# Performance work log

Measured on AMD Instinct MI355X. Metric: run time of the kernel, lower is better.

Reference implementation:

```python
import jax, jax.numpy as jnp
import numpy as np

V, H_BASE, D, L, K = 32000, 4096, 512, 2, 4
B = 64

def setup_inputs() -> dict:
    key = jax.random.key(0)
    ks = jax.random.split(key, 12)
    s = 0.02
    return {
        "hidden_state": jax.random.normal(ks[0], (B, H_BASE), jnp.float32),
        "in_proj_w": jax.random.normal(ks[1], (D, H_BASE), jnp.float32) * s,
        "in_proj_b": jnp.zeros((D,), jnp.float32),
        "w_ih0": jax.random.normal(ks[2], (3 * D, D), jnp.float32) * s,
        "w_hh0": jax.random.normal(ks[3], (3 * D, D), jnp.float32) * s,
        "b_ih0": jax.random.normal(ks[4], (3 * D,), jnp.float32) * s,
        "b_hh0": jax.random.normal(ks[5], (3 * D,), jnp.float32) * s,
        "w_ih1": jax.random.normal(ks[6], (3 * D, D), jnp.float32) * s,
        "w_hh1": jax.random.normal(ks[7], (3 * D, D), jnp.float32) * s,
        "b_ih1": jax.random.normal(ks[8], (3 * D,), jnp.float32) * s,
        "b_hh1": jax.random.normal(ks[9], (3 * D,), jnp.float32) * s,
        "embed": jax.random.normal(ks[10], (V, D), jnp.float32) * s,
        "out_w": jax.random.normal(ks[11], (V, D), jnp.float32) * s,
    }

def _gru_cell(x, h, w_ih, w_hh, b_ih, b_hh):
    # PyTorch GRU gate order: r, z, n
    gi = x @ w_ih.T + b_ih  # [B, 3D]
    gh = h @ w_hh.T + b_hh
    ir, iz, inn = jnp.split(gi, 3, axis=-1)
    hr, hz, hn = jnp.split(gh, 3, axis=-1)
    r = jax.nn.sigmoid(ir + hr)
    z = jax.nn.sigmoid(iz + hz)
    n = jnp.tanh(inn + r * hn)
    return (1.0 - z) * n + z * h

def reference(hidden_state, in_proj_w, in_proj_b, w_ih0, w_hh0, b_ih0, b_hh0,
              w_ih1, w_hh1, b_ih1, b_hh1, embed, out_w):
    b = hidden_state.shape[0]
    h0 = hidden_state @ in_proj_w.T + in_proj_b  # [B, D]
    h_l0 = h0
    h_l1 = h0
    x = jnp.zeros((b, in_proj_w.shape[0]), hidden_state.dtype)
    all_logits = []
    for _ in range(K):
        h_l0 = _gru_cell(x, h_l0, w_ih0, w_hh0, b_ih0, b_hh0)
        h_l1 = _gru_cell(h_l0, h_l1, w_ih1, w_hh1, b_ih1, b_hh1)
        logits = h_l1 @ out_w.T  # [B, V]
        all_logits.append(logits)
        x = embed[jnp.argmax(logits, axis=-1)]  # greedy next-token embed
    return jnp.stack(all_logits, axis=1)  # [B, K, V]
```

## Files before the change

kernel.cpp:

```cpp
#include <hip/hip_runtime.h>
#include <math.h>


typedef __attribute__((ext_vector_type(8))) short short8;
typedef __attribute__((ext_vector_type(4))) float f32x4;

__device__ __forceinline__ unsigned short f2bf_rne(float x) {
    unsigned u = __float_as_uint(x);
    unsigned r = (u + 0x7fffu + ((u >> 16) & 1u)) >> 16;
    return (unsigned short)r;
}
__device__ __forceinline__ void split2(float x, unsigned short& hi, unsigned short& lo) {
    unsigned u = __float_as_uint(x);
    hi = (unsigned short)(u >> 16);
    float r = x - __uint_as_float(u & 0xffff0000u);
    lo = f2bf_rne(r);
}

__device__ __forceinline__ void store_plane(unsigned short* hiP, unsigned short* loP,
                                            int m, int d, float v) {
    int s = d >> 6, cl = (d >> 3) & 7, e = d & 7;
    int off = m * 512 + s * 64 + ((cl ^ (m & 7)) * 8) + e;
    unsigned short hi, lo; split2(v, hi, lo);
    hiP[off] = hi; loP[off] = lo;
}

__device__ __forceinline__ void gload16(const void* g, void* lds) {
    __builtin_amdgcn_global_load_lds(
        (const __attribute__((address_space(1))) unsigned int*)g,
        (__attribute__((address_space(3))) unsigned int*)lds, 16, 0, 0);
}

#define LDTB 72

template<bool ARGMAX>
__device__ __forceinline__ void mfma_gemm(
    const char* __restrict__ AH, const char* __restrict__ AL, int AstrideB,
    const float* __restrict__ W, int ldbK,
    int n0, int k0, int klen,
    float* __restrict__ C, int ldc,
    unsigned short* AsH, unsigned short* AsL,
    unsigned short* BsH, unsigned short* BsL,
    float* __restrict__ pval, int* __restrict__ pidx, int bx)
{
    const int tid  = threadIdx.x;
    const int wv   = tid >> 6;
    const int lane = tid & 63;
    const int lr   = lane & 15;
    const int lh   = lane >> 4;

    f32x4 acc[4];
#pragma unroll
    for (int i = 0; i < 4; ++i) acc[i] = (f32x4){0.f, 0.f, 0.f, 0.f};

    for (int kk = k0; kk < k0 + klen; kk += 64) {
        {
            int m  = tid >> 3;
            int cp = tid & 7;
            const char* sH = AH + m * AstrideB + kk * 2 + cp * 16;
            const char* sL = AL + m * AstrideB + kk * 2 + cp * 16;
            gload16(sH, (char*)AsH + wv * 1024);
            gload16(sL, (char*)AsL + wv * 1024);
        }
#pragma unroll
        for (int r = 0; r < 4; ++r) {
            int idx = r * 512 + tid;
            int n = idx >> 4;
            int q = idx & 15;
            float4 v = *(const float4*)(W + (n0 + n) * ldbK + kk + q * 4);
            unsigned short h0,h1,h2,h3,l0,l1,l2,l3;
            split2(v.x,h0,l0); split2(v.y,h1,l1); split2(v.z,h2,l2); split2(v.w,h3,l3);
            uint2 ph = make_uint2((unsigned)h0 | ((unsigned)h1 << 16),
                                  (unsigned)h2 | ((unsigned)h3 << 16));
            uint2 pl = make_uint2((unsigned)l0 | ((unsigned)l1 << 16),
                                  (unsigned)l2 | ((unsigned)l3 << 16));
            *(uint2*)(BsH + n * LDTB + q * 4) = ph;
            *(uint2*)(BsL + n * LDTB + q * 4) = pl;
        }
        __syncthreads();

#pragma unroll
        for (int kk2 = 0; kk2 < 2; ++kk2) {
            int aoff = lr * 64 + (((kk2 * 4 + lh) ^ (lr & 7)) * 8);
            short8 ah[4], al[4];
#pragma unroll
            for (int mt = 0; mt < 4; ++mt) {
                ah[mt] = *(const short8*)(AsH + mt * 1024 + aoff);
                al[mt] = *(const short8*)(AsL + mt * 1024 + aoff);
            }
            int boff = (wv * 16 + lr) * LDTB + kk2 * 32 + lh * 8;
            short8 bh = *(const short8*)(BsH + boff);
            short8 bl = *(const short8*)(BsL + boff);
#pragma unroll
            for (int mt = 0; mt < 4; ++mt) {
                acc[mt] = __builtin_amdgcn_mfma_f32_16x16x32_bf16(ah[mt], bh, acc[mt], 0, 0, 0);
                acc[mt] = __builtin_amdgcn_mfma_f32_16x16x32_bf16(ah[mt], bl, acc[mt], 0, 0, 0);
                acc[mt] = __builtin_amdgcn_mfma_f32_16x16x32_bf16(al[mt], bh, acc[mt], 0, 0, 0);
            }
        }
        __syncthreads();
    }

#pragma unroll
    for (int mt = 0; mt < 4; ++mt)
#pragma unroll
        for (int i = 0; i < 4; ++i) {
            int m = mt * 16 + lh * 4 + i;
            C[m * ldc + n0 + wv * 16 + lr] = acc[mt][i];
        }

    if (ARGMAX) {
        float* sv = (float*)AsH;
        int*   sc = (int*)AsL;
#pragma unroll
        for (int mt = 0; mt < 4; ++mt)
#pragma unroll
            for (int i = 0; i < 4; ++i) {
                float v = acc[mt][i];
                int   c = n0 + wv * 16 + lr;
#pragma unroll
                for (int msk = 1; msk < 16; msk <<= 1) {
                    float ov = __shfl_xor(v, msk, 64);
                    int   oc = __shfl_xor(c, msk, 64);
                    if (ov > v || (ov == v && oc < c)) { v = ov; c = oc; }
                }
                if (lr == 0) {
                    int row = mt * 16 + lh * 4 + i;
                    sv[wv * 64 + row] = v;
                    sc[wv * 64 + row] = c;
                }
            }
        __syncthreads();
        if (tid < 64) {
            float v = sv[tid]; int c = sc[tid];
#pragma unroll
            for (int w = 1; w < 8; ++w) {
                float ov = sv[w * 64 + tid]; int oc = sc[w * 64 + tid];
                if (ov > v) { v = ov; c = oc; }
            }
            pval[bx * 64 + tid] = v;
            pidx[bx * 64 + tid] = c;
        }
    }
}

#define DECLARE_LDS() \
    __shared__ alignas(16) unsigned short AsH[64 * 64]; \
    __shared__ alignas(16) unsigned short AsL[64 * 64]; \
    __shared__ alignas(16) unsigned short BsH[128 * LDTB]; \
    __shared__ alignas(16) unsigned short BsL[128 * LDTB];

__global__ __launch_bounds__(256) void k_split_A(
    const float* __restrict__ hidden, char* __restrict__ hidH, char* __restrict__ hidL)
{
    int g = blockIdx.x * 256 + threadIdx.x;
    int m = g >> 9;
    int cc = g & 511;
    int s = cc >> 3, cl = cc & 7;
    const float* src = hidden + m * 4096 + cc * 8;
    float4 v0 = *(const float4*)src;
    float4 v1 = *(const float4*)(src + 4);
    unsigned short h[8], l[8];
    split2(v0.x,h[0],l[0]); split2(v0.y,h[1],l[1]); split2(v0.z,h[2],l[2]); split2(v0.w,h[3],l[3]);
    split2(v1.x,h[4],l[4]); split2(v1.y,h[5],l[5]); split2(v1.z,h[6],l[6]); split2(v1.w,h[7],l[7]);
    uint4 ph = make_uint4((unsigned)h[0]|((unsigned)h[1]<<16), (unsigned)h[2]|((unsigned)h[3]<<16),
                          (unsigned)h[4]|((unsigned)h[5]<<16), (unsigned)h[6]|((unsigned)h[7]<<16));
    uint4 pl = make_uint4((unsigned)l[0]|((unsigned)l[1]<<16), (unsigned)l[2]|((unsigned)l[3]<<16),
                          (unsigned)l[4]|((unsigned)l[5]<<16), (unsigned)l[6]|((unsigned)l[7]<<16));
    int off = m * 8192 + s * 128 + ((cl ^ (m & 7)) * 16);
    *(uint4*)(hidH + off) = ph;
    *(uint4*)(hidL + off) = pl;
}

__global__ __launch_bounds__(512) void k_inproj(
    const char* __restrict__ hidH, const char* __restrict__ hidL,
    const float* __restrict__ W, float* __restrict__ part)
{
    DECLARE_LDS();
    int nt = blockIdx.x & 3;
    int ks = blockIdx.x >> 2;
    mfma_gemm<false>(hidH, hidL, 8192, W, 4096, nt * 128, ks * 512, 512,
                     part + ks * 32768, 512, AsH, AsL, BsH, BsL, nullptr, nullptr, 0);
}

__global__ __launch_bounds__(256) void k_reduce_inproj(
    const float* __restrict__ part, const float* __restrict__ bias,
    float* __restrict__ hA, float* __restrict__ hB,
    unsigned short* hAH, unsigned short* hAL,
    unsigned short* hBH, unsigned short* hBL,
    unsigned short* xH,  unsigned short* xL)
{
    int i = blockIdx.x * 256 + threadIdx.x;
    int b = i >> 9;
    int d = i & 511;
    float s = bias[d];
#pragma unroll
    for (int ks = 0; ks < 8; ++ks) s += part[ks * 32768 + i];
    hA[i] = s;
    hB[i] = s;
    store_plane(hAH, hAL, b, d, s);
    store_plane(hBH, hBL, b, d, s);
    store_plane(xH,  xL,  b, d, 0.f);
}

__global__ __launch_bounds__(512) void k_gates(
    const char* __restrict__ xH, const char* __restrict__ xL,
    const char* __restrict__ hH, const char* __restrict__ hL,
    const float* __restrict__ w_ih, const float* __restrict__ w_hh,
    float* __restrict__ gip, float* __restrict__ ghp)
{
    DECLARE_LDS();
    int bx = blockIdx.x;
    int nt = bx % 12;
    int ks = (bx / 12) & 1;
    int mat = bx / 24;
    const char* AH = mat ? hH : xH;
    const char* AL = mat ? hL : xL;
    const float* W = mat ? w_hh : w_ih;
    float* C = (mat ? ghp : gip) + ks * 98304;
    mfma_gemm<false>(AH, AL, 1024, W, 512, nt * 128, ks * 256, 256, C, 1536,
                     AsH, AsL, BsH, BsL, nullptr, nullptr, 0);
}

__global__ __launch_bounds__(256) void k_combine(
    const float* __restrict__ gip, const float* __restrict__ ghp,
    const float* __restrict__ b_ih, const float* __restrict__ b_hh,
    float* __restrict__ h, unsigned short* hH, unsigned short* hL)
{
    int i = blockIdx.x * 256 + threadIdx.x;
    int b = i >> 9;
    int d = i & 511;
    int base = b * 1536 + d;
    float ir = gip[base]         + gip[98304 + base]         + b_ih[d];
    float iz = gip[base + 512]   + gip[98304 + base + 512]   + b_ih[d + 512];
    float inn= gip[base + 1024]  + gip[98304 + base + 1024]  + b_ih[d + 1024];
    float hr = ghp[base]         + ghp[98304 + base]         + b_hh[d];
    float hz = ghp[base + 512]   + ghp[98304 + base + 512]   + b_hh[d + 512];
    float hn = ghp[base + 1024]  + ghp[98304 + base + 1024]  + b_hh[d + 1024];
    float r = 1.f / (1.f + expf(-(ir + hr)));
    float z = 1.f / (1.f + expf(-(iz + hz)));
    float n = tanhf(inn + r * hn);
    float hv = (1.f - z) * n + z * h[i];
    h[i] = hv;
    store_plane(hH, hL, b, d, hv);
}

__global__ __launch_bounds__(512) void k_logits(
    const char* __restrict__ hH, const char* __restrict__ hL,
    const float* __restrict__ W, float* __restrict__ out, int step,
    float* __restrict__ pval, int* __restrict__ pidx)
{
    DECLARE_LDS();
    mfma_gemm<true>(hH, hL, 1024, W, 512, blockIdx.x * 128, 0, 512,
                    out + step * 32000, 128000, AsH, AsL, BsH, BsL,
                    pval, pidx, blockIdx.x);
}

__global__ __launch_bounds__(256) void k_reduce_embed(
    const float* __restrict__ pval, const int* __restrict__ pidx,
    const float* __restrict__ embed, unsigned short* xH, unsigned short* xL)
{
    __shared__ float sv[256];
    __shared__ int   sc[256];
    const int b = blockIdx.x;
    const int tid = threadIdx.x;
    float v = -3.4e38f;
    int   c = 0x7fffffff;
    if (tid < 250) { v = pval[tid * 64 + b]; c = pidx[tid * 64 + b]; }
    sv[tid] = v; sc[tid] = c;
    __syncthreads();
    for (int s = 128; s > 0; s >>= 1) {
        if (tid < s) {
            float ov = sv[tid + s]; int oc = sc[tid + s];
            if (ov > sv[tid] || (ov == sv[tid] && oc < sc[tid])) { sv[tid] = ov; sc[tid] = oc; }
        }
        __syncthreads();
    }
    int tok = sc[0];
    for (int j = tid; j < 512; j += 256)
        store_plane(xH, xL, b, j, embed[tok * 512 + j]);
}

extern "C" void kernel_launch(void* const* d_in, const int* in_sizes, int n_in,
                              void* d_out, int out_size, void* d_ws, size_t ws_size,
                              hipStream_t stream)
{
    const float* hidden = (const float*)d_in[0];
    const float* in_w   = (const float*)d_in[1];
    const float* in_b   = (const float*)d_in[2];
    const float* w_ih0  = (const float*)d_in[3];
    const float* w_hh0  = (const float*)d_in[4];
    const float* b_ih0  = (const float*)d_in[5];
    const float* b_hh0  = (const float*)d_in[6];
    const float* w_ih1  = (const float*)d_in[7];
    const float* w_hh1  = (const float*)d_in[8];
    const float* b_ih1  = (const float*)d_in[9];
    const float* b_hh1  = (const float*)d_in[10];
    const float* embed  = (const float*)d_in[11];
    const float* out_w  = (const float*)d_in[12];
    float* out = (float*)d_out;
    char*  ws  = (char*)d_ws;

    float* hA  = (float*)(ws + 0);
    float* hB  = (float*)(ws + 131072);
    unsigned short* xH  = (unsigned short*)(ws + 262144);
    unsigned short* xL  = (unsigned short*)(ws + 327680);
    unsigned short* hAH = (unsigned short*)(ws + 393216);
    unsigned short* hAL = (unsigned short*)(ws + 458752);
    unsigned short* hBH = (unsigned short*)(ws + 524288);
    unsigned short* hBL = (unsigned short*)(ws + 589824);
    char* hidH = ws + 655360;
    char* hidL = ws + 1179648;
    float* gip = (float*)(ws + 1703936);
    float* ghp = (float*)(ws + 2490368);
    float* ipart = gip;
    float* pval = (float*)(ws + 3276800);
    int*   pidx = (int*)  (ws + 3340800);

    k_split_A<<<128, 256, 0, stream>>>(hidden, hidH, hidL);
    k_inproj<<<32, 512, 0, stream>>>(hidH, hidL, in_w, ipart);
    k_reduce_inproj<<<128, 256, 0, stream>>>(ipart, in_b, hA, hB,
                                             hAH, hAL, hBH, hBL, xH, xL);

    for (int step = 0; step < 4; ++step) {
        k_gates<<<48, 512, 0, stream>>>((char*)xH, (char*)xL, (char*)hAH, (char*)hAL,
                                        w_ih0, w_hh0, gip, ghp);
        k_combine<<<128, 256, 0, stream>>>(gip, ghp, b_ih0, b_hh0, hA, hAH, hAL);
        k_gates<<<48, 512, 0, stream>>>((char*)hAH, (char*)hAL, (char*)hBH, (char*)hBL,
                                        w_ih1, w_hh1, gip, ghp);
        k_combine<<<128, 256, 0, stream>>>(gip, ghp, b_ih1, b_hh1, hB, hBH, hBL);
        k_logits<<<250, 512, 0, stream>>>((char*)hBH, (char*)hBL, out_w, out, step, pval, pidx);
        k_reduce_embed<<<64, 256, 0, stream>>>(pval, pidx, embed, xH, xL);
    }
}
```

Measured before the change: 383.7 us.

## Pre-split weights into bf16 hi/lo tiled planes and double-buffer async loads

Adds kernels that split every weight matrix (out_w, GRU weights, in_proj) into bf16 hi/lo planes once per call, stored in a pre-tiled swizzled layout. The GEMM then loads B tiles straight into LDS with async global_load_lds, in a two-stage double buffer alongside the A tiles, instead of splitting fp32 in registers on every step. The split-K factor is doubled for the GRU gates and in_proj to raise block counts. The cost is an extra upfront pass writing about 2x the weight bytes each call. After that, every logits step reads 64 MB of bf16 planes instead of 64 MB of fp32, so traffic is not reduced, only the conversion work.

```diff
diff --git a/kernel.cpp b/kernel.cpp
--- a/kernel.cpp
+++ b/kernel.cpp
@@ -31,16 +31,59 @@
         (__attribute__((address_space(3))) unsigned int*)lds, 16, 0, 0);
 }
 
-#define LDTB 72
+__device__ __forceinline__ void split_w_body(
+    const float* __restrict__ W, unsigned short* __restrict__ H,
+    unsigned short* __restrict__ L, size_t g, int kclog)
+{
+    int n  = (int)(g >> kclog);
+    int c8 = (int)g & ((1 << kclog) - 1);
+    const float* src = W + g * 8;
+    float4 v0 = *(const float4*)src;
+    float4 v1 = *(const float4*)(src + 4);
+    unsigned short h[8], l[8];
+    split2(v0.x,h[0],l[0]); split2(v0.y,h[1],l[1]); split2(v0.z,h[2],l[2]); split2(v0.w,h[3],l[3]);
+    split2(v1.x,h[4],l[4]); split2(v1.y,h[5],l[5]); split2(v1.z,h[6],l[6]); split2(v1.w,h[7],l[7]);
+    uint4 ph = make_uint4((unsigned)h[0]|((unsigned)h[1]<<16), (unsigned)h[2]|((unsigned)h[3]<<16),
+                          (unsigned)h[4]|((unsigned)h[5]<<16), (unsigned)h[6]|((unsigned)h[7]<<16));
+    uint4 pl = make_uint4((unsigned)l[0]|((unsigned)l[1]<<16), (unsigned)l[2]|((unsigned)l[3]<<16),
+                          (unsigned)l[4]|((unsigned)l[5]<<16), (unsigned)l[6]|((unsigned)l[7]<<16));
+    int nt = n >> 7, row = n & 127;
+    int ksi = c8 >> 3;
+    int slot = (c8 & 7) ^ (row & 7);
+    int tpr = 1 << (kclog - 3);
+    size_t off = ((size_t)(nt * tpr + ksi) * 128 + row) * 64 + slot * 8;
+    *(uint4*)(H + off) = ph;
+    *(uint4*)(L + off) = pl;
+}
+
+__global__ __launch_bounds__(256) void k_split_W(
+    const float* __restrict__ W, unsigned short* __restrict__ H,
+    unsigned short* __restrict__ L, int kclog)
+{
+    size_t g = (size_t)blockIdx.x * 256 + threadIdx.x;
+    split_w_body(W, H, L, g, kclog);
+}
+
+__global__ __launch_bounds__(256) void k_split_gw(
+    const float* __restrict__ w0, const float* __restrict__ w1,
+    const float* __restrict__ w2, const float* __restrict__ w3,
+    unsigned short* __restrict__ H, unsigned short* __restrict__ L)
+{
+    int mat = blockIdx.y;
+    const float* W = mat == 0 ? w0 : mat == 1 ? w1 : mat == 2 ? w2 : w3;
+    size_t g = (size_t)blockIdx.x * 256 + threadIdx.x;
+    split_w_body(W, H + (size_t)mat * 786432, L + (size_t)mat * 786432, g, 6);
+}
 
 template<bool ARGMAX>
 __device__ __forceinline__ void mfma_gemm(
-    const char* __restrict__ AH, const char* __restrict__ AL, int AstrideB,
-    const float* __restrict__ W, int ldbK,
-    int n0, int k0, int klen,
-    float* __restrict__ C, int ldc,
-    unsigned short* AsH, unsigned short* AsL,
-    unsigned short* BsH, unsigned short* BsL,
+    const char* __restrict__ AH, const char* __restrict__ AL, int AstrideB, int akk0,
+    const unsigned short* __restrict__ BH, const unsigned short* __restrict__ BL,
+    size_t btileU,
+    int nk,
+    float* __restrict__ C, int ldc, int n0,
+    unsigned short (*AsH)[4096], unsigned short (*AsL)[4096],
+    unsigned short (*BsH)[8192], unsigned short (*BsL)[8192],
     float* __restrict__ pval, int* __restrict__ pidx, int bx)
 {
     const int tid  = threadIdx.x;
@@ -48,49 +91,44 @@
     const int lane = tid & 63;
     const int lr   = lane & 15;
     const int lh   = lane >> 4;
+    const int m    = tid >> 3;
+    const int cp   = tid & 7;
 
     f32x4 acc[4];
 #pragma unroll
     for (int i = 0; i < 4; ++i) acc[i] = (f32x4){0.f, 0.f, 0.f, 0.f};
 
-    for (int kk = k0; kk < k0 + klen; kk += 64) {
-        {
-            int m  = tid >> 3;
-            int cp = tid & 7;
-            const char* sH = AH + m * AstrideB + kk * 2 + cp * 16;
-            const char* sL = AL + m * AstrideB + kk * 2 + cp * 16;
-            gload16(sH, (char*)AsH + wv * 1024);
-            gload16(sL, (char*)AsL + wv * 1024);
-        }
-#pragma unroll
-        for (int r = 0; r < 4; ++r) {
-            int idx = r * 512 + tid;
-            int n = idx >> 4;
-            int q = idx & 15;
-            float4 v = *(const float4*)(W + (n0 + n) * ldbK + kk + q * 4);
-            unsigned short h0,h1,h2,h3,l0,l1,l2,l3;
-            split2(v.x,h0,l0); split2(v.y,h1,l1); split2(v.z,h2,l2); split2(v.w,h3,l3);
-            uint2 ph = make_uint2((unsigned)h0 | ((unsigned)h1 << 16),
-                                  (unsigned)h2 | ((unsigned)h3 << 16));
-            uint2 pl = make_uint2((unsigned)l0 | ((unsigned)l1 << 16),
-                                  (unsigned)l2 | ((unsigned)l3 << 16));
-            *(uint2*)(BsH + n * LDTB + q * 4) = ph;
-            *(uint2*)(BsL + n * LDTB + q * 4) = pl;
-        }
-        __syncthreads();
-
+    auto stage = [&](int t, int p) {
+        const int ka = (akk0 + t * 64) * 2;
+        gload16(AH + m * AstrideB + ka + cp * 16, (char*)AsH[p] + wv * 1024);
+        gload16(AL + m * AstrideB + ka + cp * 16, (char*)AsL[p] + wv * 1024);
+        const char* bH = (const char*)BH + (btileU + (size_t)t * 8192) * 2;
+        const char* bL = (const char*)BL + (btileU + (size_t)t * 8192) * 2;
+        gload16(bH + wv * 2048 +        lane * 16, (char*)BsH[p] + wv * 2048);
+        gload16(bH + wv * 2048 + 1024 + lane * 16, (char*)BsH[p] + wv * 2048 + 1024);
+        gload16(bL + wv * 2048 +        lane * 16, (char*)BsL[p] + wv * 2048);
+        gload16(bL + wv * 2048 + 1024 + lane * 16, (char*)BsL[p] + wv * 2048 + 1024);
+    };
+
+    stage(0, 0);
+    __syncthreads();
+
+    for (int t = 0; t < nk; ++t) {
+        const int p = t & 1;
+        if (t + 1 < nk) stage(t + 1, p ^ 1);
 #pragma unroll
         for (int kk2 = 0; kk2 < 2; ++kk2) {
             int aoff = lr * 64 + (((kk2 * 4 + lh) ^ (lr & 7)) * 8);
             short8 ah[4], al[4];
 #pragma unroll
             for (int mt = 0; mt < 4; ++mt) {
-                ah[mt] = *(const short8*)(AsH + mt * 1024 + aoff);
-                al[mt] = *(const short8*)(AsL + mt * 1024 + aoff);
+                ah[mt] = *(const short8*)(AsH[p] + mt * 1024 + aoff);
+                al[mt] = *(const short8*)(AsL[p] + mt * 1024 + aoff);
             }
-            int boff = (wv * 16 + lr) * LDTB + kk2 * 32 + lh * 8;
-            short8 bh = *(const short8*)(BsH + boff);
-            short8 bl = *(const short8*)(BsL + boff);
+            int brow = wv * 16 + lr;
+            int boff = brow * 64 + (((kk2 * 4 + lh) ^ (brow & 7)) * 8);
+            short8 bh = *(const short8*)(BsH[p] + boff);
+            short8 bl = *(const short8*)(BsL[p] + boff);
 #pragma unroll
             for (int mt = 0; mt < 4; ++mt) {
                 acc[mt] = __builtin_amdgcn_mfma_f32_16x16x32_bf16(ah[mt], bh, acc[mt], 0, 0, 0);
@@ -105,13 +143,13 @@
     for (int mt = 0; mt < 4; ++mt)
 #pragma unroll
         for (int i = 0; i < 4; ++i) {
-            int m = mt * 16 + lh * 4 + i;
-            C[m * ldc + n0 + wv * 16 + lr] = acc[mt][i];
+            int mm = mt * 16 + lh * 4 + i;
+            C[mm * ldc + n0 + wv * 16 + lr] = acc[mt][i];
         }
 
     if (ARGMAX) {
-        float* sv = (float*)AsH;
-        int*   sc = (int*)AsL;
+        float* sv = (float*)&AsH[0][0];
+        int*   sc = (int*)&AsL[0][0];
 #pragma unroll
         for (int mt = 0; mt < 4; ++mt)
 #pragma unroll
@@ -145,10 +183,10 @@
 }
 
 #define DECLARE_LDS() \
-    __shared__ alignas(16) unsigned short AsH[64 * 64]; \
-    __shared__ alignas(16) unsigned short AsL[64 * 64]; \
-    __shared__ alignas(16) unsigned short BsH[128 * LDTB]; \
-    __shared__ alignas(16) unsigned short BsL[128 * LDTB];
+    __shared__ alignas(16) unsigned short AsH[2][4096]; \
+    __shared__ alignas(16) unsigned short AsL[2][4096]; \
+    __shared__ alignas(16) unsigned short BsH[2][8192]; \
+    __shared__ alignas(16) unsigned short BsL[2][8192];
 
 __global__ __launch_bounds__(256) void k_split_A(
     const float* __restrict__ hidden, char* __restrict__ hidH, char* __restrict__ hidL)
@@ -174,13 +212,16 @@
 
 __global__ __launch_bounds__(512) void k_inproj(
     const char* __restrict__ hidH, const char* __restrict__ hidL,
-    const float* __restrict__ W, float* __restrict__ part)
+    const unsigned short* __restrict__ WH, const unsigned short* __restrict__ WL,
+    float* __restrict__ part)
 {
     DECLARE_LDS();
     int nt = blockIdx.x & 3;
     int ks = blockIdx.x >> 2;
-    mfma_gemm<false>(hidH, hidL, 8192, W, 4096, nt * 128, ks * 512, 512,
-                     part + ks * 32768, 512, AsH, AsL, BsH, BsL, nullptr, nullptr, 0);
+    mfma_gemm<false>(hidH, hidL, 8192, ks * 256,
+                     WH, WL, (size_t)(nt * 64 + ks * 4) * 8192, 4,
+                     part + ks * 32768, 512, nt * 128,
+                     AsH, AsL, BsH, BsL, nullptr, nullptr, 0);
 }
 
 __global__ __launch_bounds__(256) void k_reduce_inproj(
@@ -195,7 +236,7 @@
     int d = i & 511;
     float s = bias[d];
 #pragma unroll
-    for (int ks = 0; ks < 8; ++ks) s += part[ks * 32768 + i];
+    for (int ks = 0; ks < 16; ++ks) s += part[ks * 32768 + i];
     hA[i] = s;
     hB[i] = s;
     store_plane(hAH, hAL, b, d, s);
@@ -206,19 +247,21 @@
 __global__ __launch_bounds__(512) void k_gates(
     const char* __restrict__ xH, const char* __restrict__ xL,
     const char* __restrict__ hH, const char* __restrict__ hL,
-    const float* __restrict__ w_ih, const float* __restrict__ w_hh,
-    float* __restrict__ gip, float* __restrict__ ghp)
+    const unsigned short* __restrict__ gwH, const unsigned short* __restrict__ gwL,
+    int layer, float* __restrict__ gip, float* __restrict__ ghp)
 {
     DECLARE_LDS();
-    int bx = blockIdx.x;
-    int nt = bx % 12;
-    int ks = (bx / 12) & 1;
-    int mat = bx / 24;
+    int bx  = blockIdx.x;
+    int nt  = bx % 12;
+    int ks  = (bx / 12) & 3;
+    int mat = bx / 48;
     const char* AH = mat ? hH : xH;
     const char* AL = mat ? hL : xL;
-    const float* W = mat ? w_hh : w_ih;
     float* C = (mat ? ghp : gip) + ks * 98304;
-    mfma_gemm<false>(AH, AL, 1024, W, 512, nt * 128, ks * 256, 256, C, 1536,
+    size_t btile = ((size_t)(layer * 2 + mat) * 96 + nt * 8 + ks * 2) * 8192;
+    mfma_gemm<false>(AH, AL, 1024, ks * 128,
+                     gwH, gwL, btile, 2,
+                     C, 1536, nt * 128,
                      AsH, AsL, BsH, BsL, nullptr, nullptr, 0);
 }
 
@@ -231,12 +274,15 @@
     int b = i >> 9;
     int d = i & 511;
     int base = b * 1536 + d;
-    float ir = gip[base]         + gip[98304 + base]         + b_ih[d];
-    float iz = gip[base + 512]   + gip[98304 + base + 512]   + b_ih[d + 512];
-    float inn= gip[base + 1024]  + gip[98304 + base + 1024]  + b_ih[d + 1024];
-    float hr = ghp[base]         + ghp[98304 + base]         + b_hh[d];
-    float hz = ghp[base + 512]   + ghp[98304 + base + 512]   + b_hh[d + 512];
-    float hn = ghp[base + 1024]  + ghp[98304 + base + 1024]  + b_hh[d + 1024];
+    float ir = b_ih[d], iz = b_ih[d + 512], inn = b_ih[d + 1024];
+    float hr = b_hh[d], hz = b_hh[d + 512], hn = b_hh[d + 1024];
+#pragma unroll
+    for (int ks = 0; ks < 4; ++ks) {
+        const float* gi = gip + ks * 98304 + base;
+        const float* gh = ghp + ks * 98304 + base;
+        ir  += gi[0];    iz += gi[512];  inn += gi[1024];
+        hr  += gh[0];    hz += gh[512];  hn  += gh[1024];
+    }
     float r = 1.f / (1.f + expf(-(ir + hr)));
     float z = 1.f / (1.f + expf(-(iz + hz)));
     float n = tanhf(inn + r * hn);
@@ -247,13 +293,15 @@
 
 __global__ __launch_bounds__(512) void k_logits(
     const char* __restrict__ hH, const char* __restrict__ hL,
-    const float* __restrict__ W, float* __restrict__ out, int step,
+    const unsigned short* __restrict__ WH, const unsigned short* __restrict__ WL,
+    float* __restrict__ out, int step,
     float* __restrict__ pval, int* __restrict__ pidx)
 {
     DECLARE_LDS();
-    mfma_gemm<true>(hH, hL, 1024, W, 512, blockIdx.x * 128, 0, 512,
-                    out + step * 32000, 128000, AsH, AsL, BsH, BsL,
-                    pval, pidx, blockIdx.x);
+    mfma_gemm<true>(hH, hL, 1024, 0,
+                    WH, WL, (size_t)blockIdx.x * 8 * 8192, 8,
+                    out + step * 32000, 128000, blockIdx.x * 128,
+                    AsH, AsL, BsH, BsL, pval, pidx, blockIdx.x);
 }
 
 __global__ __launch_bounds__(256) void k_reduce_embed(
@@ -312,24 +360,34 @@
     char* hidH = ws + 655360;
     char* hidL = ws + 1179648;
     float* gip = (float*)(ws + 1703936);
-    float* ghp = (float*)(ws + 2490368);
-    float* ipart = gip;
-    float* pval = (float*)(ws + 3276800);
-    int*   pidx = (int*)  (ws + 3340800);
+    float* ghp = (float*)(ws + 3276800);
+    float* pval = (float*)(ws + 4849664);
+    int*   pidx = (int*)  (ws + 4913664);
+    float* ipart = (float*)(ws + 4980736);
+    unsigned short* owH = (unsigned short*)(ws + 8388608);
+    unsigned short* owL = (unsigned short*)(ws + 41943040);
+    unsigned short* gwH = (unsigned short*)(ws + 75497472);
+    unsigned short* gwL = (unsigned short*)(ws + 83886080);
+    unsigned short* inH = (unsigned short*)(ws + 92274688);
+    unsigned short* inL = (unsigned short*)(ws + 96468992);
 
     k_split_A<<<128, 256, 0, stream>>>(hidden, hidH, hidL);
-    k_inproj<<<32, 512, 0, stream>>>(hidH, hidL, in_w, ipart);
+    k_split_W<<<8000, 256, 0, stream>>>(out_w, owH, owL, 6);
+    k_split_gw<<<dim3(384, 4), 256, 0, stream>>>(w_ih0, w_hh0, w_ih1, w_hh1, gwH, gwL);
+    k_split_W<<<1024, 256, 0, stream>>>(in_w, inH, inL, 9);
+    k_inproj<<<64, 512, 0, stream>>>(hidH, hidL, inH, inL, ipart);
     k_reduce_inproj<<<128, 256, 0, stream>>>(ipart, in_b, hA, hB,
                                              hAH, hAL, hBH, hBL, xH, xL);
 
     for (int step = 0; step < 4; ++step) {
-        k_gates<<<48, 512, 0, stream>>>((char*)xH, (char*)xL, (char*)hAH, (char*)hAL,
-                                        w_ih0, w_hh0, gip, ghp);
+        k_gates<<<96, 512, 0, stream>>>((char*)xH, (char*)xL, (char*)hAH, (char*)hAL,
+                                        gwH, gwL, 0, gip, ghp);
         k_combine<<<128, 256, 0, stream>>>(gip, ghp, b_ih0, b_hh0, hA, hAH, hAL);
-        k_gates<<<48, 512, 0, stream>>>((char*)hAH, (char*)hAL, (char*)hBH, (char*)hBL,
-                                        w_ih1, w_hh1, gip, ghp);
+        k_gates<<<96, 512, 0, stream>>>((char*)hAH, (char*)hAL, (char*)hBH, (char*)hBL,
+                                        gwH, gwL, 1, gip, ghp);
         k_combine<<<128, 256, 0, stream>>>(gip, ghp, b_ih1, b_hh1, hB, hBH, hBL);
-        k_logits<<<250, 512, 0, stream>>>((char*)hBH, (char*)hBL, out_w, out, step, pval, pidx);
+        k_logits<<<250, 512, 0, stream>>>((char*)hBH, (char*)hBL, owH, owL,
+                                          out, step, pval, pidx);
         k_reduce_embed<<<64, 256, 0, stream>>>(pval, pidx, embed, xH, xL);
     }
 }
```

Result: faster. 361.9 us (-5.7%).
